# Kernel optimization log

Hardware: AMD Instinct MI355X
Metric: run time of the kernel (lower is better)

Reference implementation:

```python
import jax, jax.numpy as jnp
import numpy as np

VOCAB = 100000
EMB_DIM = 50
KERNEL_NUM = 21
SIGMA = 0.1
EXACT_SIGMA = 0.001

# kernel mus/sigmas exactly as KNRM._get_kernels_layers
_MUS = [(2.0 * (i + 1) - KERNEL_NUM) / (KERNEL_NUM - 1) for i in range(KERNEL_NUM - 1)] + [1.0]
_SIGMAS = [SIGMA] * (KERNEL_NUM - 1) + [EXACT_SIGMA]


def setup_inputs() -> dict:
    key = jax.random.key(0)
    k1, k2, k3, k4, k5, k6, k7 = jax.random.split(key, 7)
    B, Lq, Ld = 1024, 32, 512
    return {
        "query_1": jax.random.randint(k1, (B, Lq), 0, VOCAB),
        "document_1": jax.random.randint(k2, (B, Ld), 0, VOCAB),
        "query_2": jax.random.randint(k3, (B, Lq), 0, VOCAB),
        "document_2": jax.random.randint(k4, (B, Ld), 0, VOCAB),
        "emb": jax.random.normal(k5, (VOCAB, EMB_DIM), dtype=jnp.float32),
        "mlp_w": jax.random.normal(k6, (1, KERNEL_NUM), dtype=jnp.float32) * 0.1,
        "mlp_b": jax.random.normal(k7, (1,), dtype=jnp.float32) * 0.1,
    }


def _predict(q_idx, d_idx, emb, mlp_w, mlp_b):
    q = emb[q_idx]                                   # [B, Lq, E]
    d = emb[d_idx]                                   # [B, Ld, E]
    qn = jnp.linalg.norm(q, axis=2)                  # [B, Lq]
    dn = jnp.linalg.norm(d, axis=2)                  # [B, Ld]
    sim = jnp.einsum('bqe,bde->bqd', q, d)
    sim = sim / (qn[:, :, None] * dn[:, None, :])
    sim = jnp.where(jnp.isnan(sim), 0.0, sim)        # [B, Lq, Ld]
    KM = []
    for mu, s in zip(_MUS, _SIGMAS):
        g = jnp.exp(-(sim - mu) ** 2 / (2.0 * s * s))
        KM.append(jnp.sum(jnp.log1p(jnp.sum(g, axis=-1)), axis=-1))
    kernels_out = jnp.stack(KM, axis=1)              # [B, 21]
    return kernels_out @ mlp_w.T + mlp_b             # [B, 1]


def reference(query_1, document_1, query_2, document_2, emb, mlp_w, mlp_b):
    logits_1 = _predict(query_1, document_1, emb, mlp_w, mlp_b)
    logits_2 = _predict(query_2, document_2, emb, mlp_w, mlp_b)
    return jax.nn.sigmoid(logits_1 - logits_2)
```

## Files before the change

kernel.cpp:

```cpp
#include <hip/hip_runtime.h>
#include <math.h>

#define LOG2E 1.4426950408889634f

typedef __attribute__((ext_vector_type(8))) short    short8;
typedef __attribute__((ext_vector_type(8))) _Float16 half8;
typedef __attribute__((ext_vector_type(4))) float    f32x4;
typedef __attribute__((ext_vector_type(2))) float    f32x2;

__device__ __forceinline__ float fexp2(float x) { return __builtin_amdgcn_exp2f(x); }

typedef __attribute__((address_space(1))) const unsigned int gas_u32;
typedef __attribute__((address_space(3))) unsigned int las_u32;
__device__ __forceinline__ void glds16(const uint4* g, uint4* l)
{ __builtin_amdgcn_global_load_lds((gas_u32*)g, (las_u32*)l, 16, 0, 0); }

__device__ __forceinline__ void kern21(f32x2 s, f32x2* acc)
{
    s.x = __builtin_amdgcn_fmed3f(s.x, -1.1f, 1.1f);
    s.y = __builtin_amdgcn_fmed3f(s.y, -1.1f, 1.1f);

    f32x2 va = s * 14.426950408889634f + 0.7213475204444817f;
    f32x2 v, vi, gc;
    v.x  = fexp2(va.x);  v.y  = fexp2(va.y);
    vi.x = __builtin_amdgcn_rcpf(v.x);
    vi.y = __builtin_amdgcn_rcpf(v.y);
    f32x2 t9 = s + 0.05f;
    f32x2 ga = (t9 * t9) * -72.13475204444817f;
    gc.x = fexp2(ga.x);  gc.y = fexp2(ga.y);

    f32x2 p = gc;
    acc[9] += p;
    #pragma unroll
    for (int k = 10; k <= 19; ++k) { p *= v; acc[k] += p; }
    f32x2 q = gc;
    #pragma unroll
    for (int k = 8; k >= 0; --k) { q *= vi; acc[k] += q; }
    if (__any(fmaxf(s.x, s.y) > 0.995f)) {
        f32x2 te = s - 1.0f;
        f32x2 ea = (te * te) * -721347.5204444817f;
        f32x2 ge; ge.x = fexp2(ea.x); ge.y = fexp2(ea.y);
        acc[20] += ge;
    }
}

__device__ __forceinline__ void doc_step2(
    half8 A0, half8 A1, half8 B0, half8 B1, f32x2* acc)
{
    f32x4 C = {0.f, 0.f, 0.f, 0.f};
    C = __builtin_amdgcn_mfma_f32_16x16x32_f16(A0, B0, C, 0, 0, 0);
    C = __builtin_amdgcn_mfma_f32_16x16x32_f16(A1, B1, C, 0, 0, 0);
    f32x2 a01 = {C[0], C[1]};
    f32x2 a23 = {C[2], C[3]};
    kern21(a01, acc);
    kern21(a23, acc);
}

__global__ __launch_bounds__(256) void knrm_prep_kernel(
    const float* __restrict__ emb, uint4* __restrict__ wse, int vocab)
{
    const int tid = threadIdx.x;
    const int row = blockIdx.x * 32 + (tid >> 3);
    const int cb  = tid & 7;
    if (row >= vocab) return;

    const float* src = emb + (size_t)row * 50;
    float v[8];
    float ss = 0.f;
    #pragma unroll
    for (int p = 0; p < 4; ++p) {
        int e = cb * 8 + 2 * p;
        float2 t;
        if (e + 2 <= 50) t = *(const float2*)(src + e);
        else             t = make_float2(0.f, 0.f);
        v[2*p]   = t.x;
        v[2*p+1] = t.y;
        ss = fmaf(t.x, t.x, fmaf(t.y, t.y, ss));
    }
    ss += __shfl_xor(ss, 1, 64);
    ss += __shfl_xor(ss, 2, 64);
    ss += __shfl_xor(ss, 4, 64);
    float rn = __builtin_amdgcn_rsqf(ss);

    half8 hv;
    #pragma unroll
    for (int p = 0; p < 8; ++p) hv[p] = (_Float16)(v[p] * rn);
    wse[(size_t)row * 8 + cb] = __builtin_bit_cast(uint4, hv);
}

__device__ __forceinline__ half8 frag_ldh(const uint4* mat, int row, int chunk)
{
    return __builtin_bit_cast(half8, mat[row * 8 + (chunk ^ (row & 7))]);
}

__global__ __launch_bounds__(256, 5) void knrm_pass_pre(
    const int* __restrict__ q1, const int* __restrict__ d1,
    const int* __restrict__ q2, const int* __restrict__ d2,
    const uint4* __restrict__ wse, const float* __restrict__ mlp_w,
    float* __restrict__ ws_logit)
{
    __shared__ uint4 dbuf[2][512];
    __shared__ float Swk[4][21][16];
    __shared__ float wred[4];

    const int tid  = threadIdx.x;
    const int bx   = blockIdx.x;
    const int b    = bx >> 1;
    const int lane = tid & 63;
    const int wave = tid >> 6;
    const int g    = lane >> 4;

    const int* qidx = ((bx & 1) ? q2 : q1) + b * 32;
    const int* didx = ((bx & 1) ? d2 : d1) + b * 512;

    const int rsub = lane >> 3;
    const int cpos = lane & 7;
    const int swz  = cpos ^ rsub;

    {
        const int srow = tid >> 3, scb = tid & 7;
        const uint4* sq = wse + (size_t)qidx[srow] * 8;
        int pos = srow * 8 + (scb ^ (srow & 7));
        dbuf[1][pos] = sq[scb];
    }
    {
        const uint4* p0 = wse + (size_t)didx[wave * 16 + rsub] * 8;
        const uint4* p1 = wse + (size_t)didx[wave * 16 + 8 + rsub] * 8;
        glds16(p0 + swz, &dbuf[0][wave * 128]);
        glds16(p1 + swz, &dbuf[0][wave * 128 + 64]);
    }
    int tokA = didx[64 + wave * 16 + rsub];
    int tokB = didx[64 + wave * 16 + 8 + rsub];
    __syncthreads();

    const int qrow = (wave >> 1) * 16 + (lane & 15);
    half8 B0 = frag_ldh(dbuf[1], qrow, g);
    half8 B1 = frag_ldh(dbuf[1], qrow, 4 + g);
    __syncthreads();

    f32x2 acc2[21];
    #pragma unroll
    for (int k = 0; k < 21; ++k) acc2[k] = (f32x2){0.f, 0.f};

    const int ar0 = (wave & 1) * 16 + (lane & 15);
    const int ar1 = 32 + ar0;

    for (int c = 0; c < 8; ++c) {
        if (c < 7) {
            const uint4* pA = wse + (size_t)tokA * 8;
            const uint4* pB = wse + (size_t)tokB * 8;
            uint4* nb = dbuf[(c + 1) & 1];
            glds16(pA + swz, nb + wave * 128);
            glds16(pB + swz, nb + wave * 128 + 64);
            if (c < 6) {
                tokA = didx[(c + 2) * 64 + wave * 16 + rsub];
                tokB = didx[(c + 2) * 64 + wave * 16 + 8 + rsub];
            }
        }
        const uint4* hb = dbuf[c & 1];
        doc_step2(frag_ldh(hb, ar0, g), frag_ldh(hb, ar0, 4 + g), B0, B1, acc2);
        doc_step2(frag_ldh(hb, ar1, g), frag_ldh(hb, ar1, 4 + g), B0, B1, acc2);
        __syncthreads();
    }

    float acc[21];
    #pragma unroll
    for (int k = 0; k < 21; ++k) {
        float v = acc2[k].x + acc2[k].y;
        v += __shfl_xor(v, 16, 64);
        v += __shfl_xor(v, 32, 64);
        acc[k] = v;
    }
    if (lane < 16) {
        #pragma unroll
        for (int k = 0; k < 21; ++k) Swk[wave][k][lane] = acc[k];
    }
    __syncthreads();

    float local = 0.f;
    for (int p = tid; p < 21 * 32; p += 256) {
        int k = p >> 5, q = p & 31;
        int wp = (q >> 4) * 2;
        float S = Swk[wp][k][q & 15] + Swk[wp + 1][k][q & 15];
        float j = (float)(k - 9);
        float scale = (k < 20) ? fexp2(-0.7213475204444817f * j * j) : 1.0f;
        local += mlp_w[k] * log1pf(S * scale);
    }
    #pragma unroll
    for (int off = 1; off < 64; off <<= 1) local += __shfl_xor(local, off, 64);
    if (lane == 0) wred[wave] = local;
    __syncthreads();
    if (tid == 0)
        ws_logit[bx] = wred[0] + wred[1] + wred[2] + wred[3];
}

__device__ __forceinline__ short8 frag_ldb(const uint4* mat, int row, int chunk)
{
    return __builtin_bit_cast(short8, mat[row * 8 + (chunk ^ (row & 7))]);
}

__device__ __forceinline__ void doc_step_fb(
    short8 Ah0, short8 Ah1, short8 Al0, short8 Al1,
    short8 Bh0, short8 Bh1, short8 Bl0, short8 Bl1, f32x2* acc)
{
    f32x4 C = {0.f, 0.f, 0.f, 0.f};
    C = __builtin_amdgcn_mfma_f32_16x16x32_bf16(Ah0, Bh0, C, 0, 0, 0);
    C = __builtin_amdgcn_mfma_f32_16x16x32_bf16(Ah1, Bh1, C, 0, 0, 0);
    C = __builtin_amdgcn_mfma_f32_16x16x32_bf16(Ah0, Bl0, C, 0, 0, 0);
    C = __builtin_amdgcn_mfma_f32_16x16x32_bf16(Ah1, Bl1, C, 0, 0, 0);
    C = __builtin_amdgcn_mfma_f32_16x16x32_bf16(Al0, Bh0, C, 0, 0, 0);
    C = __builtin_amdgcn_mfma_f32_16x16x32_bf16(Al1, Bh1, C, 0, 0, 0);
    f32x2 a01 = {C[0], C[1]};
    f32x2 a23 = {C[2], C[3]};
    kern21(a01, acc);
    kern21(a23, acc);
}

__device__ __forceinline__ void stage_row_chunk(
    const float* __restrict__ emb, int tok, int row, int cb,
    uint4* __restrict__ hmat, uint4* __restrict__ lmat)
{
    const float* src = emb + (size_t)tok * 50;
    float v[8];
    float ss = 0.f;
    #pragma unroll
    for (int p = 0; p < 4; ++p) {
        int e = cb * 8 + 2 * p;
        float2 t;
        if (e + 2 <= 50) t = *(const float2*)(src + e);
        else             t = make_float2(0.f, 0.f);
        v[2*p]   = t.x;
        v[2*p+1] = t.y;
        ss = fmaf(t.x, t.x, fmaf(t.y, t.y, ss));
    }
    ss += __shfl_xor(ss, 1, 64);
    ss += __shfl_xor(ss, 2, 64);
    ss += __shfl_xor(ss, 4, 64);
    float rn = __builtin_amdgcn_rsqf(ss);

    unsigned hw[4], lw[4];
    #pragma unroll
    for (int p = 0; p < 4; ++p) {
        float a = v[2*p]   * rn;
        float b = v[2*p+1] * rn;
        unsigned ha = __float_as_uint(a) & 0xFFFF0000u;
        unsigned hb = __float_as_uint(b) & 0xFFFF0000u;
        float la = a - __uint_as_float(ha);
        float lb = b - __uint_as_float(hb);
        hw[p] = (ha >> 16) | hb;
        lw[p] = (__float_as_uint(la) >> 16) | (__float_as_uint(lb) & 0xFFFF0000u);
    }
    int cidx = cb ^ (row & 7);
    hmat[row * 8 + cidx] = make_uint4(hw[0], hw[1], hw[2], hw[3]);
    lmat[row * 8 + cidx] = make_uint4(lw[0], lw[1], lw[2], lw[3]);
}

__global__ __launch_bounds__(256, 4) void knrm_pass_fb(
    const int* __restrict__ q1, const int* __restrict__ d1,
    const int* __restrict__ q2, const int* __restrict__ d2,
    const float* __restrict__ emb, const float* __restrict__ mlp_w,
    float* __restrict__ ws_logit)
{
    __shared__ uint4 qh4[256], ql4[256];
    __shared__ uint4 dh4[256], dl4[256];
    __shared__ float Swk[4][21][16];
    __shared__ float wred[4];

    const int tid  = threadIdx.x;
    const int bx   = blockIdx.x;
    const int b    = bx >> 1;
    const int lane = tid & 63;
    const int wave = tid >> 6;
    const int g    = lane >> 4;

    const int* qidx = ((bx & 1) ? q2 : q1) + b * 32;
    const int* didx = ((bx & 1) ? d2 : d1) + b * 512;

    const int srow = tid >> 3;
    const int scb  = tid & 7;

    stage_row_chunk(emb, qidx[srow], srow, scb, qh4, ql4);
    __syncthreads();

    const int qrow = (wave >> 1) * 16 + (lane & 15);
    short8 Bh0 = frag_ldb(qh4, qrow, g);
    short8 Bh1 = frag_ldb(qh4, qrow, 4 + g);
    short8 Bl0 = frag_ldb(ql4, qrow, g);
    short8 Bl1 = frag_ldb(ql4, qrow, 4 + g);

    f32x2 acc2[21];
    #pragma unroll
    for (int k = 0; k < 21; ++k) acc2[k] = (f32x2){0.f, 0.f};

    const int arow = (wave & 1) * 16 + (lane & 15);

    for (int c = 0; c < 16; ++c) {
        if (c) __syncthreads();
        stage_row_chunk(emb, didx[c * 32 + srow], srow, scb, dh4, dl4);
        __syncthreads();
        doc_step_fb(frag_ldb(dh4, arow, g), frag_ldb(dh4, arow, 4 + g),
                    frag_ldb(dl4, arow, g), frag_ldb(dl4, arow, 4 + g),
                    Bh0, Bh1, Bl0, Bl1, acc2);
    }
    __syncthreads();

    float acc[21];
    #pragma unroll
    for (int k = 0; k < 21; ++k) {
        float v = acc2[k].x + acc2[k].y;
        v += __shfl_xor(v, 16, 64);
        v += __shfl_xor(v, 32, 64);
        acc[k] = v;
    }
    if (lane < 16) {
        #pragma unroll
        for (int k = 0; k < 21; ++k) Swk[wave][k][lane] = acc[k];
    }
    __syncthreads();

    float local = 0.f;
    for (int p = tid; p < 21 * 32; p += 256) {
        int k = p >> 5, q = p & 31;
        int wp = (q >> 4) * 2;
        float S = Swk[wp][k][q & 15] + Swk[wp + 1][k][q & 15];
        float j = (float)(k - 9);
        float scale = (k < 20) ? fexp2(-0.7213475204444817f * j * j) : 1.0f;
        local += mlp_w[k] * log1pf(S * scale);
    }
    #pragma unroll
    for (int off = 1; off < 64; off <<= 1) local += __shfl_xor(local, off, 64);
    if (lane == 0) wred[wave] = local;
    __syncthreads();
    if (tid == 0)
        ws_logit[bx] = wred[0] + wred[1] + wred[2] + wred[3];
}

__global__ void knrm_final_kernel(const float* __restrict__ P,
                                  float* __restrict__ out, int B)
{
    int i = blockIdx.x * 256 + threadIdx.x;
    if (i < B) {
        float x = P[2 * i] - P[2 * i + 1];
        out[i] = 1.0f / (1.0f + fexp2(-LOG2E * x));
    }
}

extern "C" void kernel_launch(void* const* d_in, const int* in_sizes, int n_in,
                              void* d_out, int out_size, void* d_ws, size_t ws_size,
                              hipStream_t stream) {
    const int*   q1    = (const int*)d_in[0];
    const int*   d1    = (const int*)d_in[1];
    const int*   q2    = (const int*)d_in[2];
    const int*   d2    = (const int*)d_in[3];
    const float* emb   = (const float*)d_in[4];
    const float* mlp_w = (const float*)d_in[5];
    float*       out   = (float*)d_out;

    const int B     = out_size;
    const int vocab = in_sizes[4] / 50;

    float* ws_logit = (float*)d_ws;
    uint4* wse      = (uint4*)((char*)d_ws + 8192);
    size_t need     = 8192 + (size_t)vocab * 128;

    if (ws_size >= need) {
        knrm_prep_kernel<<<dim3((vocab + 31) / 32), dim3(256), 0, stream>>>(emb, wse, vocab);
        knrm_pass_pre<<<dim3(2 * B), dim3(256), 0, stream>>>(
            q1, d1, q2, d2, wse, mlp_w, ws_logit);
    } else {
        knrm_pass_fb<<<dim3(2 * B), dim3(256), 0, stream>>>(
            q1, d1, q2, d2, emb, mlp_w, ws_logit);
    }
    knrm_final_kernel<<<dim3((B + 255) / 256), dim3(256), 0, stream>>>(ws_logit, out, B);
}
```

Measured before the change: 61.15 us.

## Triple-buffer document gathers with partial vmcnt waits and LDS-staged indices

Moves the document embedding gather ring from two LDS buffers to three, prefetching two chunks ahead. The full __syncthreads at each step becomes a partial s_waitcnt vmcnt plus s_barrier, so later loads can stay in flight while the current chunk is processed. Document token indices are staged in LDS once instead of being re-read from global memory in the loop, and the loop is fully unrolled. This adds LDS footprint, which may lower occupancy under launch_bounds(256,5), and relies on hand-managed waitcnt counts being correct.

```diff
diff --git a/kernel.cpp b/kernel.cpp
--- a/kernel.cpp
+++ b/kernel.cpp
@@ -14,6 +14,14 @@
 typedef __attribute__((address_space(3))) unsigned int las_u32;
 __device__ __forceinline__ void glds16(const uint4* g, uint4* l)
 { __builtin_amdgcn_global_load_lds((gas_u32*)g, (las_u32*)l, 16, 0, 0); }
+
+#define WAIT_BARRIER(N)                                          \
+    do {                                                         \
+        asm volatile("s_waitcnt vmcnt(" #N ")" ::: "memory");    \
+        __builtin_amdgcn_sched_barrier(0);                       \
+        __builtin_amdgcn_s_barrier();                            \
+        __builtin_amdgcn_sched_barrier(0);                       \
+    } while (0)
 
 __device__ __forceinline__ void kern21(f32x2 s, f32x2* acc)
 {
@@ -99,7 +107,8 @@
     const uint4* __restrict__ wse, const float* __restrict__ mlp_w,
     float* __restrict__ ws_logit)
 {
-    __shared__ uint4 dbuf[2][512];
+    __shared__ uint4 dbuf[3][512];
+    __shared__ int   didxL[512];
     __shared__ float Swk[4][21][16];
     __shared__ float wred[4];
 
@@ -117,26 +126,33 @@
     const int cpos = lane & 7;
     const int swz  = cpos ^ rsub;
 
+    didxL[tid]       = didx[tid];
+    didxL[256 + tid] = didx[256 + tid];
     {
         const int srow = tid >> 3, scb = tid & 7;
         const uint4* sq = wse + (size_t)qidx[srow] * 8;
         int pos = srow * 8 + (scb ^ (srow & 7));
-        dbuf[1][pos] = sq[scb];
+        dbuf[2][pos] = sq[scb];
     }
     {
         const uint4* p0 = wse + (size_t)didx[wave * 16 + rsub] * 8;
         const uint4* p1 = wse + (size_t)didx[wave * 16 + 8 + rsub] * 8;
         glds16(p0 + swz, &dbuf[0][wave * 128]);
         glds16(p1 + swz, &dbuf[0][wave * 128 + 64]);
-    }
-    int tokA = didx[64 + wave * 16 + rsub];
-    int tokB = didx[64 + wave * 16 + 8 + rsub];
+        const uint4* pa = wse + (size_t)didx[64 + wave * 16 + rsub] * 8;
+        const uint4* pb = wse + (size_t)didx[64 + wave * 16 + 8 + rsub] * 8;
+        glds16(pa + swz, &dbuf[1][wave * 128]);
+        glds16(pb + swz, &dbuf[1][wave * 128 + 64]);
+    }
     __syncthreads();
 
     const int qrow = (wave >> 1) * 16 + (lane & 15);
-    half8 B0 = frag_ldh(dbuf[1], qrow, g);
-    half8 B1 = frag_ldh(dbuf[1], qrow, 4 + g);
-    __syncthreads();
+    half8 B0 = frag_ldh(dbuf[2], qrow, g);
+    half8 B1 = frag_ldh(dbuf[2], qrow, 4 + g);
+    __syncthreads();
+
+    int tokA = didxL[128 + wave * 16 + rsub];
+    int tokB = didxL[128 + wave * 16 + 8 + rsub];
 
     f32x2 acc2[21];
     #pragma unroll
@@ -145,22 +161,34 @@
     const int ar0 = (wave & 1) * 16 + (lane & 15);
     const int ar1 = 32 + ar0;
 
-    for (int c = 0; c < 8; ++c) {
-        if (c < 7) {
+    #pragma unroll
+    for (int c = 0; c < 6; ++c) {
+        {
             const uint4* pA = wse + (size_t)tokA * 8;
             const uint4* pB = wse + (size_t)tokB * 8;
-            uint4* nb = dbuf[(c + 1) & 1];
+            uint4* nb = dbuf[(c + 2) % 3];
             glds16(pA + swz, nb + wave * 128);
             glds16(pB + swz, nb + wave * 128 + 64);
-            if (c < 6) {
-                tokA = didx[(c + 2) * 64 + wave * 16 + rsub];
-                tokB = didx[(c + 2) * 64 + wave * 16 + 8 + rsub];
-            }
         }
-        const uint4* hb = dbuf[c & 1];
+        if (c < 5) {
+            tokA = didxL[(c + 3) * 64 + wave * 16 + rsub];
+            tokB = didxL[(c + 3) * 64 + wave * 16 + 8 + rsub];
+        }
+        const uint4* hb = dbuf[c % 3];
         doc_step2(frag_ldh(hb, ar0, g), frag_ldh(hb, ar0, 4 + g), B0, B1, acc2);
         doc_step2(frag_ldh(hb, ar1, g), frag_ldh(hb, ar1, 4 + g), B0, B1, acc2);
-        __syncthreads();
+        WAIT_BARRIER(2);
+    }
+    {
+        const uint4* hb = dbuf[6 % 3];
+        doc_step2(frag_ldh(hb, ar0, g), frag_ldh(hb, ar0, 4 + g), B0, B1, acc2);
+        doc_step2(frag_ldh(hb, ar1, g), frag_ldh(hb, ar1, 4 + g), B0, B1, acc2);
+        WAIT_BARRIER(0);
+    }
+    {
+        const uint4* hb = dbuf[7 % 3];
+        doc_step2(frag_ldh(hb, ar0, g), frag_ldh(hb, ar0, 4 + g), B0, B1, acc2);
+        doc_step2(frag_ldh(hb, ar1, g), frag_ldh(hb, ar1, 4 + g), B0, B1, acc2);
     }
 
     float acc[21];
```

After: 64.80 us. +6.0%, slower.
